# Kernel tuning notes

Measured on AMD Instinct MI355X. Metric: run time of the kernel, lower is better.

The kernel has to match this reference:

```python
import math
import jax, jax.numpy as jnp
import numpy as np

B, S, IN_DIM, D_MODEL, L, T_Y = 16, 512, 64, 64, 32, 256
T_X = T_Y + L - 1
RIDGE = 0.01
THRESH = 0.005


def _pos_encoding(seq_len, d):
    pos = jnp.arange(seq_len, dtype=jnp.float32)[:, None]
    div = jnp.exp(jnp.arange(0, d, 2, dtype=jnp.float32) * (-(math.log(10000.0) / d)))
    ang = pos * div  # [S, d/2]
    pe = jnp.zeros((seq_len, d), dtype=jnp.float32)
    pe = pe.at[:, 0::2].set(jnp.sin(ang)).at[:, 1::2].set(jnp.cos(ang))
    return pe


def _layernorm(h, gamma, beta, eps=1e-5):
    mu = jnp.mean(h, axis=-1, keepdims=True)
    var = jnp.mean((h - mu) ** 2, axis=-1, keepdims=True)
    return (h - mu) * jax.lax.rsqrt(var + eps) * gamma + beta


def setup_inputs() -> dict:
    key = jax.random.key(0)
    ks = jax.random.split(key, 8)
    return {
        "fps": jax.random.normal(ks[0], (B, S, IN_DIM), dtype=jnp.float32),
        "x": jax.random.normal(ks[1], (B, S, T_X), dtype=jnp.float32),
        "y": jax.random.normal(ks[2], (B, S, T_Y), dtype=jnp.float32),
        "sample_steps": jax.random.randint(ks[3], (5,), 10, S),
        "W1": jax.random.normal(ks[4], (IN_DIM, 256), dtype=jnp.float32) / math.sqrt(IN_DIM),
        "b1": jnp.zeros((256,), dtype=jnp.float32),
        "gamma": jnp.ones((256,), dtype=jnp.float32),
        "beta": jnp.zeros((256,), dtype=jnp.float32),
        "W2": jax.random.normal(ks[5], (256, D_MODEL), dtype=jnp.float32) / math.sqrt(256.0),
        "b2": jnp.zeros((D_MODEL,), dtype=jnp.float32),
        "Wq": jax.random.normal(ks[6], (D_MODEL, D_MODEL), dtype=jnp.float32) / math.sqrt(D_MODEL),
        "bq": jnp.zeros((D_MODEL,), dtype=jnp.float32),
        "Wk": jax.random.normal(ks[7], (D_MODEL, D_MODEL), dtype=jnp.float32) / math.sqrt(D_MODEL),
        "bk": jnp.zeros((D_MODEL,), dtype=jnp.float32),
    }


def reference(fps, x, y, sample_steps, W1, b1, gamma, beta, W2, b2, Wq, bq, Wk, bk):
    batch, seq_len, _ = fps.shape
    d = Wq.shape[0]
    t_y = y.shape[-1]
    filt = x.shape[-1] - t_y + 1  # L

    # encoder: Linear -> LayerNorm -> Tanh -> Linear -> Tanh
    h = _layernorm(fps @ W1 + b1, gamma, beta)
    e_orig = jnp.tanh(jnp.tanh(h) @ W2 + b2)  # [B,S,d]
    e = e_orig + 0.05 * _pos_encoding(seq_len, d)[None]

    q = e @ Wq + bq
    k = e @ Wk + bk
    scores = jnp.einsum('bsd,btd->bst', q, k) / math.sqrt(d)
    causal = jnp.triu(jnp.ones((seq_len, seq_len), dtype=bool), 1)
    scores = jnp.where(causal[None], -1e9, scores)
    alpha = jax.nn.softmax(scores * 2.0, axis=-1)  # [B,S,S]

    # sliding windows: X[b,s] = unfold(x[b,s], L, 1)[:T_y] -> [T_y, L]
    win = jnp.arange(t_y)[:, None] + jnp.arange(filt)[None, :]
    X = x[:, :, win]  # [B,S,T_y,L]

    # per-source gram / cross contributions
    G = jnp.einsum('bstl,bstm->bslm', X, X)  # [B,S,L,L]
    C = jnp.einsum('bstl,bst->bsl', X, y)    # [B,S,L]

    w = alpha[:, sample_steps, :]            # [B,T,S]
    wm = jnp.where(w > THRESH, w, 0.0)

    gram = jnp.einsum('bts,bslm->btlm', wm, G) + RIDGE * jnp.eye(filt, dtype=x.dtype)
    cross = jnp.einsum('bts,bsl->btl', wm, C)
    wt_hat = jnp.linalg.solve(gram, cross[..., None])[..., 0]  # [B,T,L]

    Xt = X[:, sample_steps]  # [B,T,T_y,L]
    yt = y[:, sample_steps]  # [B,T,T_y]
    pred = jnp.einsum('btkl,btl->btk', Xt, wt_hat)
    loss_bt = jnp.mean((yt - pred) ** 2, axis=-1)  # [B,T]

    valid = jnp.any(wm > 0.0, axis=-1)  # [B,T]
    total = jnp.sum(jnp.where(valid, loss_bt, 0.0))
    n = jnp.maximum(jnp.sum(valid.astype(jnp.int32)), 1)
    loss = total / n
    return loss, alpha, e_orig
```

## Files before the change

kernel.cpp:

```cpp
#include <hip/hip_runtime.h>
#include <hip/hip_bf16.h>
#include <math.h>

#define BB 16
#define SS 512
#define INDIM 64
#define DMODEL 64
#define HID 256
#define FILT 32
#define TYY 256
#define TXX 287
#define NT 5
#define RIDGEF 0.01f
#define THRESHF 0.005f
#define GRAMN 1088
#define GRAMTOT (BB * NT * GRAMN)

__global__ __launch_bounds__(256) void k_mlp(
    const float* __restrict__ fps, const float* __restrict__ W1, const float* __restrict__ b1,
    const float* __restrict__ gamma, const float* __restrict__ beta,
    const float* __restrict__ W2, const float* __restrict__ b2,
    const float* __restrict__ Wq, const float* __restrict__ bq,
    const float* __restrict__ Wk, const float* __restrict__ bk,
    float* __restrict__ e_out, float* __restrict__ q_out, float* __restrict__ kT_out,
    float* __restrict__ gram, int* __restrict__ ctrs)
{
    const int row0 = blockIdx.x << 3;
    const int tid = threadIdx.x;
    const int wid = tid >> 6, lane = tid & 63;

    if (blockIdx.x < GRAMTOT / 256) {
        gram[(size_t)blockIdx.x * 256 + tid] = 0.f;
    } else if (blockIdx.x == GRAMTOT / 256 && tid < 4) {
        ctrs[tid] = 0;
    }

    __shared__ float fr[8][INDIM];
    __shared__ float th4[8][HID];
    __shared__ float ee4[4][DMODEL];
    __shared__ float part4[4][4][DMODEL];
    __shared__ float partk4[4][4][DMODEL];
    __shared__ float wred[4][8][2];

    { int r = tid >> 6, i = tid & 63;
      fr[r][i]     = fps[(row0 + r) * INDIM + i];
      fr[r + 4][i] = fps[(row0 + r + 4) * INDIM + i]; }
    __syncthreads();

    float h[8];
    float b1v = b1[tid];
    #pragma unroll
    for (int r = 0; r < 8; ++r) h[r] = b1v;
    for (int i = 0; i < INDIM; ++i) {
        float w = W1[i * HID + tid];
        #pragma unroll
        for (int r = 0; r < 8; ++r) h[r] = fmaf(fr[r][i], w, h[r]);
    }

    float s1[8], s2[8];
    #pragma unroll
    for (int r = 0; r < 8; ++r) { s1[r] = h[r]; s2[r] = h[r] * h[r]; }
    #pragma unroll
    for (int off = 1; off < 64; off <<= 1) {
        #pragma unroll
        for (int r = 0; r < 8; ++r) {
            s1[r] += __shfl_xor(s1[r], off);
            s2[r] += __shfl_xor(s2[r], off);
        }
    }
    if (lane == 0) {
        #pragma unroll
        for (int r = 0; r < 8; ++r) { wred[wid][r][0] = s1[r]; wred[wid][r][1] = s2[r]; }
    }
    __syncthreads();
    float gm = gamma[tid], bt = beta[tid];
    #pragma unroll
    for (int r = 0; r < 8; ++r) {
        float t1 = wred[0][r][0] + wred[1][r][0] + wred[2][r][0] + wred[3][r][0];
        float t2 = wred[0][r][1] + wred[1][r][1] + wred[2][r][1] + wred[3][r][1];
        float mu = t1 * (1.0f / HID);
        float var = t2 * (1.0f / HID) - mu * mu;
        float hn = (h[r] - mu) * rsqrtf(var + 1e-5f) * gm + bt;
        th4[r][tid] = tanhf(hn);
    }
    __syncthreads();

    #pragma unroll
    for (int half = 0; half < 2; ++half) {
        const int rbase = half * 4;
        { int p = tid >> 6, j = tid & 63;
          float acc[4] = {0.f, 0.f, 0.f, 0.f};
          for (int i = p * 64; i < p * 64 + 64; ++i) {
              float w = W2[i * DMODEL + j];
              #pragma unroll
              for (int r = 0; r < 4; ++r) acc[r] = fmaf(th4[rbase + r][i], w, acc[r]);
          }
          #pragma unroll
          for (int r = 0; r < 4; ++r) part4[p][r][j] = acc[r];
        }
        __syncthreads();
        { int r = tid >> 6, j = tid & 63;
          float e = part4[0][r][j] + part4[1][r][j] + part4[2][r][j] + part4[3][r][j] + b2[j];
          float eo = tanhf(e);
          int row = row0 + rbase + r;
          int s = row & (SS - 1);
          e_out[(size_t)row * DMODEL + j] = eo;
          float div = expf(-(float)(j & ~1) * 0.14391156831212787f);
          float ang = (float)s * div;
          float pe = (j & 1) ? cosf(ang) : sinf(ang);
          ee4[r][j] = eo + 0.05f * pe;
        }
        __syncthreads();
        { int p = tid >> 6, j = tid & 63;
          float aq[4] = {0.f,0.f,0.f,0.f}, ak[4] = {0.f,0.f,0.f,0.f};
          for (int i = p * 16; i < p * 16 + 16; ++i) {
              float wqv = Wq[i * DMODEL + j];
              float wkv = Wk[i * DMODEL + j];
              #pragma unroll
              for (int r = 0; r < 4; ++r) {
                  aq[r] = fmaf(ee4[r][i], wqv, aq[r]);
                  ak[r] = fmaf(ee4[r][i], wkv, ak[r]);
              }
          }
          #pragma unroll
          for (int r = 0; r < 4; ++r) { part4[p][r][j] = aq[r]; partk4[p][r][j] = ak[r]; }
        }
        __syncthreads();
        { int r = tid >> 6, j = tid & 63;
          float qv = part4[0][r][j] + part4[1][r][j] + part4[2][r][j] + part4[3][r][j] + bq[j];
          float kv = partk4[0][r][j] + partk4[1][r][j] + partk4[2][r][j] + partk4[3][r][j] + bk[j];
          int row = row0 + rbase + r;
          int b = row >> 9, s = row & (SS - 1);
          q_out[(size_t)row * DMODEL + j] = qv;
          kT_out[(size_t)(b * DMODEL + j) * SS + s] = kv;
        }
        __syncthreads();
    }
}

__global__ __launch_bounds__(256) void k_attn(
    const float* __restrict__ q, const float* __restrict__ kT,
    float* __restrict__ alpha)
{
    const int blk = blockIdx.x;
    const int b = blk >> 7;
    const int t0 = (blk & 127) << 2;
    const int t3 = t0 + 3;
    const int tid = threadIdx.x;
    const int wave = tid >> 6, lane = tid & 63;

    __shared__ float qt[4 * DMODEL];
    __shared__ float redm[4][4];

    qt[tid] = q[(size_t)(b * SS + t0 + (tid >> 6)) * DMODEL + (tid & 63)];
    __syncthreads();

    const float* kTb = kT + (size_t)b * DMODEL * SS;
    const int s0 = tid, s1 = tid + 256;
    float a0[4] = {0,0,0,0}, a1[4] = {0,0,0,0};
    if (s1 <= t3) {
        for (int d = 0; d < DMODEL; ++d) {
            float k0 = kTb[d * SS + s0];
            float k1 = kTb[d * SS + s1];
            #pragma unroll
            for (int r = 0; r < 4; ++r) {
                float qv = qt[r * DMODEL + d];
                a0[r] = fmaf(qv, k0, a0[r]);
                a1[r] = fmaf(qv, k1, a1[r]);
            }
        }
    } else if (s0 <= t3) {
        for (int d = 0; d < DMODEL; ++d) {
            float k0 = kTb[d * SS + s0];
            #pragma unroll
            for (int r = 0; r < 4; ++r) a0[r] = fmaf(qt[r * DMODEL + d], k0, a0[r]);
        }
    }
    float lg0[4], lg1[4];
    #pragma unroll
    for (int r = 0; r < 4; ++r) {
        int tr = t0 + r;
        lg0[r] = (s0 <= tr) ? 0.25f * a0[r] : -INFINITY;
        lg1[r] = (s1 <= tr) ? 0.25f * a1[r] : -INFINITY;
    }
    float mr[4];
    #pragma unroll
    for (int r = 0; r < 4; ++r) {
        float m = fmaxf(lg0[r], lg1[r]);
        #pragma unroll
        for (int off = 32; off > 0; off >>= 1) m = fmaxf(m, __shfl_xor(m, off));
        if (lane == 0) redm[r][wave] = m;
    }
    __syncthreads();
    #pragma unroll
    for (int r = 0; r < 4; ++r)
        mr[r] = fmaxf(fmaxf(redm[r][0], redm[r][1]), fmaxf(redm[r][2], redm[r][3]));
    __syncthreads();
    float ex0[4], ex1[4], sr[4];
    #pragma unroll
    for (int r = 0; r < 4; ++r) {
        ex0[r] = expf(lg0[r] - mr[r]);
        ex1[r] = expf(lg1[r] - mr[r]);
        float sm = ex0[r] + ex1[r];
        #pragma unroll
        for (int off = 32; off > 0; off >>= 1) sm += __shfl_xor(sm, off);
        if (lane == 0) redm[r][wave] = sm;
    }
    __syncthreads();
    #pragma unroll
    for (int r = 0; r < 4; ++r)
        sr[r] = redm[r][0] + redm[r][1] + redm[r][2] + redm[r][3];
    #pragma unroll
    for (int r = 0; r < 4; ++r) {
        float inv = 1.0f / sr[r];
        size_t base = (size_t)(b * SS + t0 + r) * SS;
        alpha[base + s0] = ex0[r] * inv;
        alpha[base + s1] = ex1[r] * inv;
    }
}

__global__ __launch_bounds__(256) void k_gpart(
    const float* __restrict__ x, const float* __restrict__ y,
    const int* __restrict__ steps, const float* __restrict__ alpha,
    float* __restrict__ gram, int C, int CS)
{
    const int b = blockIdx.x / C;
    const int chunk = blockIdx.x % C;
    const int tid = threadIdx.x;
    const int lane = tid & 63, wid = tid >> 6;

    __shared__ __align__(16) float xs[288];
    __shared__ __align__(16) float ys[256];
    __shared__ float Gs[1056];
    __shared__ float crossL[32];
    __shared__ float wv[NT * 64];
    __shared__ float wtot[NT];
    __shared__ int sl[64];
    __shared__ int nselS;
    __shared__ int stS[NT];
    __shared__ float redA[4][33];
    __shared__ float redB[4][33];

    if (tid < NT) stS[tid] = steps[tid];
    if (tid < 32) Gs[tid * 33 + 32] = 0.f;
    __syncthreads();

    for (int idx = tid; idx < NT * CS; idx += 256) {
        int t = idx / CS, si = idx % CS;
        float a = alpha[(size_t)(b * SS + stS[t]) * SS + chunk * CS + si];
        wv[t * 64 + si] = (a > THRESHF) ? a : 0.f;
    }
    __syncthreads();
    if (tid < NT) {
        float s = 0.f;
        for (int si = 0; si < CS; ++si) s += wv[tid * 64 + si];
        wtot[tid] = s;
    }
    if (wid == 0) {
        float m = 0.f;
        if (lane < CS)
            m = wv[lane] + wv[64 + lane] + wv[128 + lane] + wv[192 + lane] + wv[256 + lane];
        unsigned long long mask = __ballot(m > 0.f);
        if (m > 0.f) {
            int pos = __popcll(mask & ((1ull << lane) - 1ull));
            sl[pos] = lane;
        }
        if (lane == 0) nselS = __popcll(mask);
    }
    __syncthreads();
    const int nsel = nselS;

    float acc[NT][5];
    #pragma unroll
    for (int t = 0; t < NT; ++t) {
        #pragma unroll
        for (int r = 0; r < 5; ++r) acc[t][r] = 0.f;
    }

    float rx0 = 0.f, rx1 = 0.f, ry = 0.f;
    if (nsel > 0) {
        int sg = chunk * CS + sl[0];
        const float* xr = x + (size_t)(b * SS + sg) * TXX;
        const float* yr = y + (size_t)(b * SS + sg) * TYY;
        rx0 = xr[tid];
        if (tid < 31) rx1 = xr[256 + tid];
        ry = yr[tid];
    }

    for (int i = 0; i < nsel; ++i) {
        xs[tid] = rx0;
        if (tid < 31) xs[256 + tid] = rx1;
        ys[tid] = ry;
        const int sl_cur = sl[i];
        __syncthreads();

        if (i + 1 < nsel) {
            int sg = chunk * CS + sl[i + 1];
            const float* xr = x + (size_t)(b * SS + sg) * TXX;
            const float* yr = y + (size_t)(b * SS + sg) * TYY;
            rx0 = xr[tid];
            if (tid < 31) rx1 = xr[256 + tid];
            ry = yr[tid];
        }

        { int l = tid & 31, p = tid >> 5;
          const float4* xk4 = (const float4*)(xs + (p << 5));
          const float4* yk4 = (const float4*)(ys + (p << 5));
          float c = 0.f, a = 0.f;
          #pragma unroll
          for (int j = 0; j < 8; ++j) {
              float4 xk = xk4[j];
              float4 yk = yk4[j];
              int kb = (p << 5) + (j << 2);
              float x0 = xs[kb + l],     x1 = xs[kb + 1 + l];
              float x2 = xs[kb + 2 + l], x3 = xs[kb + 3 + l];
              c = fmaf(x0, yk.x, c); a = fmaf(xk.x, x0, a);
              c = fmaf(x1, yk.y, c); a = fmaf(xk.y, x1, a);
              c = fmaf(x2, yk.z, c); a = fmaf(xk.z, x2, a);
              c = fmaf(x3, yk.w, c); a = fmaf(xk.w, x3, a);
          }
          c += __shfl_xor(c, 32);
          a += __shfl_xor(a, 32);
          if (lane < 32) { redA[wid][l] = c; redB[wid][l] = a; }
        }
        __syncthreads();

        if (tid < 32)
            crossL[tid] = redA[0][tid] + redA[1][tid] + redA[2][tid] + redA[3][tid];

        { int jj = lane & 31;
          #pragma unroll
          for (int pass = 0; pass < 4; ++pass) {
              int dd = 2 * (wid + 4 * pass) + (lane >> 5);
              float g0 = redB[0][dd] + redB[1][dd] + redB[2][dd] + redB[3][dd];
              float dlt = 0.f;
              if (jj > 0 && jj + dd < 32)
                  dlt = xs[jj + 255] * xs[jj + 255 + dd]
                      - xs[jj - 1] * xs[jj - 1 + dd];
              #pragma unroll
              for (int off = 1; off < 32; off <<= 1) {
                  float tsh = __shfl_up(dlt, off, 32);
                  if (jj >= off) dlt += tsh;
              }
              if (jj + dd < 32) {
                  float gval = g0 + dlt;
                  Gs[jj * 33 + jj + dd] = gval;
                  Gs[(jj + dd) * 33 + jj] = gval;
              }
          }
        }
        __syncthreads();

        { float g0 = Gs[tid], g1 = Gs[tid + 256], g2 = Gs[tid + 512], g3 = Gs[tid + 768];
          float g4 = (tid < 32) ? Gs[1024 + tid]
                   : ((tid < 64) ? crossL[tid - 32] : 0.f);
          #pragma unroll
          for (int t = 0; t < NT; ++t) {
              float w = wv[t * 64 + sl_cur];
              if (w > 0.f) {
                  acc[t][0] = fmaf(w, g0, acc[t][0]);
                  acc[t][1] = fmaf(w, g1, acc[t][1]);
                  acc[t][2] = fmaf(w, g2, acc[t][2]);
                  acc[t][3] = fmaf(w, g3, acc[t][3]);
                  acc[t][4] = fmaf(w, g4, acc[t][4]);
              }
          }
        }
    }

    #pragma unroll
    for (int t = 0; t < NT; ++t) {
        if (wtot[t] > 0.f) {
            float* gr = gram + (size_t)(b * NT + t) * GRAMN;
            #pragma unroll
            for (int r = 0; r < 4; ++r) atomicAdd(&gr[tid + 256 * r], acc[t][r]);
            if (tid < 64) atomicAdd(&gr[1024 + tid], acc[t][4]);
        }
    }
}

__global__ __launch_bounds__(256) void k_solve2(
    const float* __restrict__ x, const float* __restrict__ y,
    const int* __restrict__ steps, const float* __restrict__ alpha,
    const float* __restrict__ gram,
    int* __restrict__ ctrs, float* __restrict__ out0)
{
    const int g = blockIdx.x;
    const int b = g / NT, t = g % NT;
    const int tid = threadIdx.x;

    __shared__ float Af[1056];
    __shared__ float zs[FILT];
    __shared__ float wt[FILT];
    __shared__ float xsr[TXX + 1];
    __shared__ float red[256];
    __shared__ int step_s;
    __shared__ int anyv;

    if (tid == 0) { step_s = steps[t]; anyv = 0; }
    __syncthreads();

    const float* row = gram + (size_t)g * GRAMN;
    Af[tid] = row[tid];
    Af[tid + 256] = row[tid + 256];
    Af[tid + 512] = row[tid + 512];
    Af[tid + 768] = row[tid + 768];
    if (tid < 32) Af[1024 + tid] = row[1024 + tid];
    else if (tid < 64) zs[tid - 32] = row[1024 + tid];

    { const float* arow = alpha + (size_t)(b * SS + step_s) * SS;
      if (arow[tid] > THRESHF || arow[tid + 256] > THRESHF) anyv = 1; }
    __syncthreads();
    if (tid < 32) Af[tid * 33 + tid] += RIDGEF;
    __syncthreads();

    if (tid < 32) {
        float a[32];
        #pragma unroll
        for (int j = 0; j < 32; ++j) a[j] = Af[tid * 33 + j];
        #pragma unroll
        for (int k = 0; k < 32; ++k) {
            float akk = __shfl(a[k], k);
            float dk = sqrtf(akk);
            float ck = a[k] / dk;
            if (tid >= k) a[k] = ck;
            #pragma unroll
            for (int m = k + 1; m < 32; ++m) {
                float cm = __shfl(ck, m);
                if (tid >= m) a[m] = fmaf(-ck, cm, a[m]);
            }
        }
        #pragma unroll
        for (int j = 0; j < 32; ++j)
            if (j <= tid) Af[tid * 33 + j] = a[j];

        float zl = zs[tid];
        #pragma unroll
        for (int k = 0; k < 32; ++k) {
            float akk = __shfl(a[k], k);
            float zk = __shfl(zl, k) / akk;
            if (tid == k) zl = zk;
            else if (tid > k) zl = fmaf(-a[k], zk, zl);
        }
        #pragma unroll
        for (int k = 31; k >= 0; --k) {
            float akk = __shfl(a[k], k);
            float wk = __shfl(zl, k) / akk;
            if (tid == k) zl = wk;
            else if (tid < k) zl = fmaf(-Af[k * 33 + tid], wk, zl);
        }
        wt[tid] = zl;
    }
    __syncthreads();

    const int sstep = step_s;
    const float* xrow = x + (size_t)(b * SS + sstep) * TXX;
    for (int i = tid; i < TXX; i += 256) xsr[i] = xrow[i];
    __syncthreads();
    float pk = 0.f;
    #pragma unroll
    for (int l = 0; l < FILT; ++l) pk = fmaf(xsr[tid + l], wt[l], pk);
    float d = y[(size_t)(b * SS + sstep) * TYY + tid] - pk;
    red[tid] = d * d;
    __syncthreads();
    for (int off = 128; off > 0; off >>= 1) {
        if (tid < off) red[tid] += red[tid + off];
        __syncthreads();
    }
    if (tid == 0) {
        float lossval = red[0] * (1.0f / TYY);
        float* loss_sum = (float*)(ctrs + 2);
        if (anyv) {
            atomicAdd(loss_sum, lossval);
            atomicAdd(&ctrs[1], 1);
        }
        __threadfence();
        int prev = atomicAdd(&ctrs[0], 1);
        if (prev == BB * NT - 1) {
            float s = atomicAdd(loss_sum, 0.0f);
            int c = atomicAdd(&ctrs[1], 0);
            out0[0] = s / (float)(c > 0 ? c : 1);
        }
    }
}

extern "C" void kernel_launch(void* const* d_in, const int* in_sizes, int n_in,
                              void* d_out, int out_size, void* d_ws, size_t ws_size,
                              hipStream_t stream)
{
    const float* fps  = (const float*)d_in[0];
    const float* x    = (const float*)d_in[1];
    const float* y    = (const float*)d_in[2];
    const int* steps  = (const int*)d_in[3];
    const float* W1   = (const float*)d_in[4];
    const float* b1   = (const float*)d_in[5];
    const float* gamma= (const float*)d_in[6];
    const float* beta = (const float*)d_in[7];
    const float* W2   = (const float*)d_in[8];
    const float* b2   = (const float*)d_in[9];
    const float* Wq   = (const float*)d_in[10];
    const float* bq   = (const float*)d_in[11];
    const float* Wk   = (const float*)d_in[12];
    const float* bk   = (const float*)d_in[13];

    float* out   = (float*)d_out;
    float* alpha = out + 1;
    float* e_out = out + 1 + (size_t)BB * SS * SS;

    float* gram = (float*)d_ws;
    int*   ctrs = (int*)(gram + GRAMTOT);
    float* q    = (float*)(ctrs + 4);
    float* kT   = q + (size_t)BB * SS * DMODEL;

    const int C = 64, CS = SS / 64;

    hipLaunchKernelGGL(k_mlp, dim3(BB * SS / 8), dim3(256), 0, stream,
                       fps, W1, b1, gamma, beta, W2, b2, Wq, bq, Wk, bk,
                       e_out, q, kT, gram, ctrs);
    hipLaunchKernelGGL(k_attn, dim3(BB * (SS / 4)), dim3(256), 0, stream,
                       q, kT, alpha);
    hipLaunchKernelGGL(k_gpart, dim3(BB * C), dim3(256), 0, stream,
                       x, y, steps, alpha, gram, C, CS);
    hipLaunchKernelGGL(k_solve2, dim3(BB * NT), dim3(256), 0, stream,
                       x, y, steps, alpha, gram, ctrs, out);
}
```

Measured before the change: 200.2 us.

## Fuse all stages into one persistent kernel with software grid barriers

Merges the MLP, attention, gram-accumulation and solve kernels into a single persistent kernel of 448 blocks. Each block loops over work units, and the stages are separated by atomic-counter grid barriers. Zeroing of the gram buffer, counters and barriers moves to a hipMemsetAsync. The aim is to remove inter-kernel launch gaps and tail effects, at the cost of spin-wait barriers, a fixed grid that must fit co-resident (launch bounds 256,2), and a union of shared-memory layouts.

```diff
diff --git a/kernel.cpp b/kernel.cpp
--- a/kernel.cpp
+++ b/kernel.cpp
@@ -1,5 +1,4 @@
 #include <hip/hip_runtime.h>
-#include <hip/hip_bf16.h>
 #include <math.h>
 
 #define BB 16
@@ -15,287 +14,294 @@
 #define THRESHF 0.005f
 #define GRAMN 1088
 #define GRAMTOT (BB * NT * GRAMN)
-
-__global__ __launch_bounds__(256) void k_mlp(
-    const float* __restrict__ fps, const float* __restrict__ W1, const float* __restrict__ b1,
+#define NBLK 448
+
+union __align__(16) SharedU {
+    struct {
+        float fr[8][INDIM];
+        float th4[8][HID];
+        float ee4[4][DMODEL];
+        float part4[4][4][DMODEL];
+        float partk4[4][4][DMODEL];
+        float wred[4][8][2];
+    } m;
+    struct {
+        float qt[4 * DMODEL];
+        float redm[4][4];
+    } a;
+    struct {
+        float xs[288];
+        float ys[256];
+        float Gs[1056];
+        float crossL[32];
+        float wv[NT * 64];
+        float wtot[NT];
+        int sl[64];
+        int nselS;
+        int stS[NT];
+        float redA[4][33];
+        float redB[4][33];
+    } g;
+    struct {
+        float Af[1056];
+        float zs[FILT];
+        float wt[FILT];
+        float xsr[TXX + 1];
+        float red[256];
+    } s;
+};
+
+__device__ __forceinline__ void grid_barrier(int* bar2, int nblocks)
+{
+    __syncthreads();
+    if (threadIdx.x == 0) {
+        __threadfence();
+        if (atomicAdd(&bar2[0], 1) == nblocks - 1) {
+            atomicExch(&bar2[1], 1);
+        } else {
+            while (atomicAdd(&bar2[1], 0) == 0) __builtin_amdgcn_s_sleep(8);
+        }
+        __threadfence();
+    }
+    __syncthreads();
+}
+
+__global__ __launch_bounds__(256, 2) void k_fused(
+    const float* __restrict__ fps, const float* __restrict__ x,
+    const float* __restrict__ y, const int* __restrict__ steps,
+    const float* __restrict__ W1, const float* __restrict__ b1,
     const float* __restrict__ gamma, const float* __restrict__ beta,
     const float* __restrict__ W2, const float* __restrict__ b2,
     const float* __restrict__ Wq, const float* __restrict__ bq,
     const float* __restrict__ Wk, const float* __restrict__ bk,
-    float* __restrict__ e_out, float* __restrict__ q_out, float* __restrict__ kT_out,
-    float* __restrict__ gram, int* __restrict__ ctrs)
+    float* __restrict__ e_out, float* __restrict__ alpha,
+    float* __restrict__ q_out, float* __restrict__ kT_out,
+    float* __restrict__ gram, int* __restrict__ ctrs, int* __restrict__ bars,
+    float* __restrict__ out0)
 {
-    const int row0 = blockIdx.x << 3;
+    __shared__ SharedU su;
     const int tid = threadIdx.x;
     const int wid = tid >> 6, lane = tid & 63;
 
-    if (blockIdx.x < GRAMTOT / 256) {
-        gram[(size_t)blockIdx.x * 256 + tid] = 0.f;
-    } else if (blockIdx.x == GRAMTOT / 256 && tid < 4) {
-        ctrs[tid] = 0;
+    for (int u = blockIdx.x; u < BB * SS / 8; u += NBLK) {
+        const int row0 = u << 3;
+        { int r = tid >> 6, i = tid & 63;
+          su.m.fr[r][i]     = fps[(row0 + r) * INDIM + i];
+          su.m.fr[r + 4][i] = fps[(row0 + r + 4) * INDIM + i]; }
+        __syncthreads();
+
+        float h[8];
+        float b1v = b1[tid];
+        #pragma unroll
+        for (int r = 0; r < 8; ++r) h[r] = b1v;
+        for (int i = 0; i < INDIM; ++i) {
+            float w = W1[i * HID + tid];
+            #pragma unroll
+            for (int r = 0; r < 8; ++r) h[r] = fmaf(su.m.fr[r][i], w, h[r]);
+        }
+
+        float s1[8], s2[8];
+        #pragma unroll
+        for (int r = 0; r < 8; ++r) { s1[r] = h[r]; s2[r] = h[r] * h[r]; }
+        #pragma unroll
+        for (int off = 1; off < 64; off <<= 1) {
+            #pragma unroll
+            for (int r = 0; r < 8; ++r) {
+                s1[r] += __shfl_xor(s1[r], off);
+                s2[r] += __shfl_xor(s2[r], off);
+            }
+        }
+        if (lane == 0) {
+            #pragma unroll
+            for (int r = 0; r < 8; ++r) { su.m.wred[wid][r][0] = s1[r]; su.m.wred[wid][r][1] = s2[r]; }
+        }
+        __syncthreads();
+        float gm = gamma[tid], bt = beta[tid];
+        #pragma unroll
+        for (int r = 0; r < 8; ++r) {
+            float t1 = su.m.wred[0][r][0] + su.m.wred[1][r][0] + su.m.wred[2][r][0] + su.m.wred[3][r][0];
+            float t2 = su.m.wred[0][r][1] + su.m.wred[1][r][1] + su.m.wred[2][r][1] + su.m.wred[3][r][1];
+            float mu = t1 * (1.0f / HID);
+            float var = t2 * (1.0f / HID) - mu * mu;
+            float hn = (h[r] - mu) * rsqrtf(var + 1e-5f) * gm + bt;
+            su.m.th4[r][tid] = tanhf(hn);
+        }
+        __syncthreads();
+
+        #pragma unroll
+        for (int half = 0; half < 2; ++half) {
+            const int rbase = half * 4;
+            { int p = tid >> 6, j = tid & 63;
+              float acc[4] = {0.f, 0.f, 0.f, 0.f};
+              for (int i = p * 64; i < p * 64 + 64; ++i) {
+                  float w = W2[i * DMODEL + j];
+                  #pragma unroll
+                  for (int r = 0; r < 4; ++r) acc[r] = fmaf(su.m.th4[rbase + r][i], w, acc[r]);
+              }
+              #pragma unroll
+              for (int r = 0; r < 4; ++r) su.m.part4[p][r][j] = acc[r];
+            }
+            __syncthreads();
+            { int r = tid >> 6, j = tid & 63;
+              float e = su.m.part4[0][r][j] + su.m.part4[1][r][j] + su.m.part4[2][r][j] + su.m.part4[3][r][j] + b2[j];
+              float eo = tanhf(e);
+              int row = row0 + rbase + r;
+              int s = row & (SS - 1);
+              e_out[(size_t)row * DMODEL + j] = eo;
+              float div = expf(-(float)(j & ~1) * 0.14391156831212787f);
+              float ang = (float)s * div;
+              float pe = (j & 1) ? cosf(ang) : sinf(ang);
+              su.m.ee4[r][j] = eo + 0.05f * pe;
+            }
+            __syncthreads();
+            { int p = tid >> 6, j = tid & 63;
+              float aq[4] = {0.f,0.f,0.f,0.f}, ak[4] = {0.f,0.f,0.f,0.f};
+              for (int i = p * 16; i < p * 16 + 16; ++i) {
+                  float wqv = Wq[i * DMODEL + j];
+                  float wkv = Wk[i * DMODEL + j];
+                  #pragma unroll
+                  for (int r = 0; r < 4; ++r) {
+                      aq[r] = fmaf(su.m.ee4[r][i], wqv, aq[r]);
+                      ak[r] = fmaf(su.m.ee4[r][i], wkv, ak[r]);
+                  }
+              }
+              #pragma unroll
+              for (int r = 0; r < 4; ++r) { su.m.part4[p][r][j] = aq[r]; su.m.partk4[p][r][j] = ak[r]; }
+            }
+            __syncthreads();
+            { int r = tid >> 6, j = tid & 63;
+              float qv = su.m.part4[0][r][j] + su.m.part4[1][r][j] + su.m.part4[2][r][j] + su.m.part4[3][r][j] + bq[j];
+              float kv = su.m.partk4[0][r][j] + su.m.partk4[1][r][j] + su.m.partk4[2][r][j] + su.m.partk4[3][r][j] + bk[j];
+              int row = row0 + rbase + r;
+              int b = row >> 9, s = row & (SS - 1);
+              q_out[(size_t)row * DMODEL + j] = qv;
+              kT_out[(size_t)(b * DMODEL + j) * SS + s] = kv;
+            }
+            __syncthreads();
+        }
     }
-
-    __shared__ float fr[8][INDIM];
-    __shared__ float th4[8][HID];
-    __shared__ float ee4[4][DMODEL];
-    __shared__ float part4[4][4][DMODEL];
-    __shared__ float partk4[4][4][DMODEL];
-    __shared__ float wred[4][8][2];
-
-    { int r = tid >> 6, i = tid & 63;
-      fr[r][i]     = fps[(row0 + r) * INDIM + i];
-      fr[r + 4][i] = fps[(row0 + r + 4) * INDIM + i]; }
-    __syncthreads();
-
-    float h[8];
-    float b1v = b1[tid];
-    #pragma unroll
-    for (int r = 0; r < 8; ++r) h[r] = b1v;
-    for (int i = 0; i < INDIM; ++i) {
-        float w = W1[i * HID + tid];
-        #pragma unroll
-        for (int r = 0; r < 8; ++r) h[r] = fmaf(fr[r][i], w, h[r]);
+    grid_barrier(bars + 0, NBLK);
+
+    for (int u = blockIdx.x; u < BB * (SS / 4); u += NBLK) {
+        const int b = u >> 7;
+        const int t0 = (u & 127) << 2;
+        const int t3 = t0 + 3;
+
+        su.a.qt[tid] = q_out[(size_t)(b * SS + t0 + (tid >> 6)) * DMODEL + (tid & 63)];
+        __syncthreads();
+
+        const float* kTb = kT_out + (size_t)b * DMODEL * SS;
+        const int s0 = tid, s1 = tid + 256;
+        float a0[4] = {0,0,0,0}, a1[4] = {0,0,0,0};
+        if (s1 <= t3) {
+            for (int d = 0; d < DMODEL; ++d) {
+                float k0 = kTb[d * SS + s0];
+                float k1 = kTb[d * SS + s1];
+                #pragma unroll
+                for (int r = 0; r < 4; ++r) {
+                    float qv = su.a.qt[r * DMODEL + d];
+                    a0[r] = fmaf(qv, k0, a0[r]);
+                    a1[r] = fmaf(qv, k1, a1[r]);
+                }
+            }
+        } else if (s0 <= t3) {
+            for (int d = 0; d < DMODEL; ++d) {
+                float k0 = kTb[d * SS + s0];
+                #pragma unroll
+                for (int r = 0; r < 4; ++r) a0[r] = fmaf(su.a.qt[r * DMODEL + d], k0, a0[r]);
+            }
+        }
+        float lg0[4], lg1[4];
+        #pragma unroll
+        for (int r = 0; r < 4; ++r) {
+            int tr = t0 + r;
+            lg0[r] = (s0 <= tr) ? 0.25f * a0[r] : -INFINITY;
+            lg1[r] = (s1 <= tr) ? 0.25f * a1[r] : -INFINITY;
+        }
+        float mr[4];
+        #pragma unroll
+        for (int r = 0; r < 4; ++r) {
+            float m = fmaxf(lg0[r], lg1[r]);
+            #pragma unroll
+            for (int off = 32; off > 0; off >>= 1) m = fmaxf(m, __shfl_xor(m, off));
+            if (lane == 0) su.a.redm[r][wid] = m;
+        }
+        __syncthreads();
+        #pragma unroll
+        for (int r = 0; r < 4; ++r)
+            mr[r] = fmaxf(fmaxf(su.a.redm[r][0], su.a.redm[r][1]),
+                          fmaxf(su.a.redm[r][2], su.a.redm[r][3]));
+        __syncthreads();
+        float ex0[4], ex1[4], sr[4];
+        #pragma unroll
+        for (int r = 0; r < 4; ++r) {
+            ex0[r] = expf(lg0[r] - mr[r]);
+            ex1[r] = expf(lg1[r] - mr[r]);
+            float sm = ex0[r] + ex1[r];
+            #pragma unroll
+            for (int off = 32; off > 0; off >>= 1) sm += __shfl_xor(sm, off);
+            if (lane == 0) su.a.redm[r][wid] = sm;
+        }
+        __syncthreads();
+        #pragma unroll
+        for (int r = 0; r < 4; ++r)
+            sr[r] = su.a.redm[r][0] + su.a.redm[r][1] + su.a.redm[r][2] + su.a.redm[r][3];
+        #pragma unroll
+        for (int r = 0; r < 4; ++r) {
+            float inv = 1.0f / sr[r];
+            size_t base = (size_t)(b * SS + t0 + r) * SS;
+            alpha[base + s0] = ex0[r] * inv;
+            alpha[base + s1] = ex1[r] * inv;
+        }
+        __syncthreads();
     }
-
-    float s1[8], s2[8];
-    #pragma unroll
-    for (int r = 0; r < 8; ++r) { s1[r] = h[r]; s2[r] = h[r] * h[r]; }
-    #pragma unroll
-    for (int off = 1; off < 64; off <<= 1) {
-        #pragma unroll
-        for (int r = 0; r < 8; ++r) {
-            s1[r] += __shfl_xor(s1[r], off);
-            s2[r] += __shfl_xor(s2[r], off);
-        }
-    }
-    if (lane == 0) {
-        #pragma unroll
-        for (int r = 0; r < 8; ++r) { wred[wid][r][0] = s1[r]; wred[wid][r][1] = s2[r]; }
-    }
-    __syncthreads();
-    float gm = gamma[tid], bt = beta[tid];
-    #pragma unroll
-    for (int r = 0; r < 8; ++r) {
-        float t1 = wred[0][r][0] + wred[1][r][0] + wred[2][r][0] + wred[3][r][0];
-        float t2 = wred[0][r][1] + wred[1][r][1] + wred[2][r][1] + wred[3][r][1];
-        float mu = t1 * (1.0f / HID);
-        float var = t2 * (1.0f / HID) - mu * mu;
-        float hn = (h[r] - mu) * rsqrtf(var + 1e-5f) * gm + bt;
-        th4[r][tid] = tanhf(hn);
-    }
-    __syncthreads();
-
-    #pragma unroll
-    for (int half = 0; half < 2; ++half) {
-        const int rbase = half * 4;
-        { int p = tid >> 6, j = tid & 63;
-          float acc[4] = {0.f, 0.f, 0.f, 0.f};
-          for (int i = p * 64; i < p * 64 + 64; ++i) {
-              float w = W2[i * DMODEL + j];
-              #pragma unroll
-              for (int r = 0; r < 4; ++r) acc[r] = fmaf(th4[rbase + r][i], w, acc[r]);
-          }
-          #pragma unroll
-          for (int r = 0; r < 4; ++r) part4[p][r][j] = acc[r];
-        }
-        __syncthreads();
-        { int r = tid >> 6, j = tid & 63;
-          float e = part4[0][r][j] + part4[1][r][j] + part4[2][r][j] + part4[3][r][j] + b2[j];
-          float eo = tanhf(e);
-          int row = row0 + rbase + r;
-          int s = row & (SS - 1);
-          e_out[(size_t)row * DMODEL + j] = eo;
-          float div = expf(-(float)(j & ~1) * 0.14391156831212787f);
-          float ang = (float)s * div;
-          float pe = (j & 1) ? cosf(ang) : sinf(ang);
-          ee4[r][j] = eo + 0.05f * pe;
-        }
-        __syncthreads();
-        { int p = tid >> 6, j = tid & 63;
-          float aq[4] = {0.f,0.f,0.f,0.f}, ak[4] = {0.f,0.f,0.f,0.f};
-          for (int i = p * 16; i < p * 16 + 16; ++i) {
-              float wqv = Wq[i * DMODEL + j];
-              float wkv = Wk[i * DMODEL + j];
-              #pragma unroll
-              for (int r = 0; r < 4; ++r) {
-                  aq[r] = fmaf(ee4[r][i], wqv, aq[r]);
-                  ak[r] = fmaf(ee4[r][i], wkv, ak[r]);
-              }
-          }
-          #pragma unroll
-          for (int r = 0; r < 4; ++r) { part4[p][r][j] = aq[r]; partk4[p][r][j] = ak[r]; }
-        }
-        __syncthreads();
-        { int r = tid >> 6, j = tid & 63;
-          float qv = part4[0][r][j] + part4[1][r][j] + part4[2][r][j] + part4[3][r][j] + bq[j];
-          float kv = partk4[0][r][j] + partk4[1][r][j] + partk4[2][r][j] + partk4[3][r][j] + bk[j];
-          int row = row0 + rbase + r;
-          int b = row >> 9, s = row & (SS - 1);
-          q_out[(size_t)row * DMODEL + j] = qv;
-          kT_out[(size_t)(b * DMODEL + j) * SS + s] = kv;
-        }
-        __syncthreads();
-    }
-}
-
-__global__ __launch_bounds__(256) void k_attn(
-    const float* __restrict__ q, const float* __restrict__ kT,
-    float* __restrict__ alpha)
-{
-    const int blk = blockIdx.x;
-    const int b = blk >> 7;
-    const int t0 = (blk & 127) << 2;
-    const int t3 = t0 + 3;
-    const int tid = threadIdx.x;
-    const int wave = tid >> 6, lane = tid & 63;
-
-    __shared__ float qt[4 * DMODEL];
-    __shared__ float redm[4][4];
-
-    qt[tid] = q[(size_t)(b * SS + t0 + (tid >> 6)) * DMODEL + (tid & 63)];
-    __syncthreads();
-
-    const float* kTb = kT + (size_t)b * DMODEL * SS;
-    const int s0 = tid, s1 = tid + 256;
-    float a0[4] = {0,0,0,0}, a1[4] = {0,0,0,0};
-    if (s1 <= t3) {
-        for (int d = 0; d < DMODEL; ++d) {
-            float k0 = kTb[d * SS + s0];
-            float k1 = kTb[d * SS + s1];
-            #pragma unroll
-            for (int r = 0; r < 4; ++r) {
-                float qv = qt[r * DMODEL + d];
-                a0[r] = fmaf(qv, k0, a0[r]);
-                a1[r] = fmaf(qv, k1, a1[r]);
-            }
-        }
-    } else if (s0 <= t3) {
-        for (int d = 0; d < DMODEL; ++d) {
-            float k0 = kTb[d * SS + s0];
-            #pragma unroll
-            for (int r = 0; r < 4; ++r) a0[r] = fmaf(qt[r * DMODEL + d], k0, a0[r]);
-        }
-    }
-    float lg0[4], lg1[4];
-    #pragma unroll
-    for (int r = 0; r < 4; ++r) {
-        int tr = t0 + r;
-        lg0[r] = (s0 <= tr) ? 0.25f * a0[r] : -INFINITY;
-        lg1[r] = (s1 <= tr) ? 0.25f * a1[r] : -INFINITY;
-    }
-    float mr[4];
-    #pragma unroll
-    for (int r = 0; r < 4; ++r) {
-        float m = fmaxf(lg0[r], lg1[r]);
-        #pragma unroll
-        for (int off = 32; off > 0; off >>= 1) m = fmaxf(m, __shfl_xor(m, off));
-        if (lane == 0) redm[r][wave] = m;
-    }
-    __syncthreads();
-    #pragma unroll
-    for (int r = 0; r < 4; ++r)
-        mr[r] = fmaxf(fmaxf(redm[r][0], redm[r][1]), fmaxf(redm[r][2], redm[r][3]));
-    __syncthreads();
-    float ex0[4], ex1[4], sr[4];
-    #pragma unroll
-    for (int r = 0; r < 4; ++r) {
-        ex0[r] = expf(lg0[r] - mr[r]);
-        ex1[r] = expf(lg1[r] - mr[r]);
-        float sm = ex0[r] + ex1[r];
-        #pragma unroll
-        for (int off = 32; off > 0; off >>= 1) sm += __shfl_xor(sm, off);
-        if (lane == 0) redm[r][wave] = sm;
-    }
-    __syncthreads();
-    #pragma unroll
-    for (int r = 0; r < 4; ++r)
-        sr[r] = redm[r][0] + redm[r][1] + redm[r][2] + redm[r][3];
-    #pragma unroll
-    for (int r = 0; r < 4; ++r) {
-        float inv = 1.0f / sr[r];
-        size_t base = (size_t)(b * SS + t0 + r) * SS;
-        alpha[base + s0] = ex0[r] * inv;
-        alpha[base + s1] = ex1[r] * inv;
-    }
-}
-
-__global__ __launch_bounds__(256) void k_gpart(
-    const float* __restrict__ x, const float* __restrict__ y,
-    const int* __restrict__ steps, const float* __restrict__ alpha,
-    float* __restrict__ gram, int C, int CS)
-{
-    const int b = blockIdx.x / C;
-    const int chunk = blockIdx.x % C;
-    const int tid = threadIdx.x;
-    const int lane = tid & 63, wid = tid >> 6;
-
-    __shared__ __align__(16) float xs[288];
-    __shared__ __align__(16) float ys[256];
-    __shared__ float Gs[1056];
-    __shared__ float crossL[32];
-    __shared__ float wv[NT * 64];
-    __shared__ float wtot[NT];
-    __shared__ int sl[64];
-    __shared__ int nselS;
-    __shared__ int stS[NT];
-    __shared__ float redA[4][33];
-    __shared__ float redB[4][33];
-
-    if (tid < NT) stS[tid] = steps[tid];
-    if (tid < 32) Gs[tid * 33 + 32] = 0.f;
-    __syncthreads();
-
-    for (int idx = tid; idx < NT * CS; idx += 256) {
-        int t = idx / CS, si = idx % CS;
-        float a = alpha[(size_t)(b * SS + stS[t]) * SS + chunk * CS + si];
-        wv[t * 64 + si] = (a > THRESHF) ? a : 0.f;
-    }
-    __syncthreads();
-    if (tid < NT) {
-        float s = 0.f;
-        for (int si = 0; si < CS; ++si) s += wv[tid * 64 + si];
-        wtot[tid] = s;
-    }
-    if (wid == 0) {
-        float m = 0.f;
-        if (lane < CS)
-            m = wv[lane] + wv[64 + lane] + wv[128 + lane] + wv[192 + lane] + wv[256 + lane];
-        unsigned long long mask = __ballot(m > 0.f);
-        if (m > 0.f) {
-            int pos = __popcll(mask & ((1ull << lane) - 1ull));
-            sl[pos] = lane;
-        }
-        if (lane == 0) nselS = __popcll(mask);
-    }
-    __syncthreads();
-    const int nsel = nselS;
-
-    float acc[NT][5];
-    #pragma unroll
-    for (int t = 0; t < NT; ++t) {
-        #pragma unroll
-        for (int r = 0; r < 5; ++r) acc[t][r] = 0.f;
-    }
-
-    float rx0 = 0.f, rx1 = 0.f, ry = 0.f;
-    if (nsel > 0) {
-        int sg = chunk * CS + sl[0];
-        const float* xr = x + (size_t)(b * SS + sg) * TXX;
-        const float* yr = y + (size_t)(b * SS + sg) * TYY;
-        rx0 = xr[tid];
-        if (tid < 31) rx1 = xr[256 + tid];
-        ry = yr[tid];
-    }
-
-    for (int i = 0; i < nsel; ++i) {
-        xs[tid] = rx0;
-        if (tid < 31) xs[256 + tid] = rx1;
-        ys[tid] = ry;
-        const int sl_cur = sl[i];
-        __syncthreads();
-
-        if (i + 1 < nsel) {
-            int sg = chunk * CS + sl[i + 1];
+    grid_barrier(bars + 2, NBLK);
+
+    const int C = 64, CS = SS / 64;
+    for (int u = blockIdx.x; u < BB * C; u += NBLK) {
+        const int b = u / C;
+        const int chunk = u % C;
+
+        if (tid < NT) su.g.stS[tid] = steps[tid];
+        if (tid < 32) su.g.Gs[tid * 33 + 32] = 0.f;
+        __syncthreads();
+
+        for (int idx = tid; idx < NT * CS; idx += 256) {
+            int t = idx / CS, si = idx % CS;
+            float a = alpha[(size_t)(b * SS + su.g.stS[t]) * SS + chunk * CS + si];
+            su.g.wv[t * 64 + si] = (a > THRESHF) ? a : 0.f;
+        }
+        __syncthreads();
+        if (tid < NT) {
+            float s = 0.f;
+            for (int si = 0; si < CS; ++si) s += su.g.wv[tid * 64 + si];
+            su.g.wtot[tid] = s;
+        }
+        if (wid == 0) {
+            float m = 0.f;
+            if (lane < CS)
+                m = su.g.wv[lane] + su.g.wv[64 + lane] + su.g.wv[128 + lane]
+                  + su.g.wv[192 + lane] + su.g.wv[256 + lane];
+            unsigned long long mask = __ballot(m > 0.f);
+            if (m > 0.f) {
+                int pos = __popcll(mask & ((1ull << lane) - 1ull));
+                su.g.sl[pos] = lane;
+            }
+            if (lane == 0) su.g.nselS = __popcll(mask);
+        }
+        __syncthreads();
+        const int nsel = su.g.nselS;
+
+        float acc[NT][5];
+        #pragma unroll
+        for (int t = 0; t < NT; ++t) {
+            #pragma unroll
+            for (int r = 0; r < 5; ++r) acc[t][r] = 0.f;
+        }
+
+        float rx0 = 0.f, rx1 = 0.f, ry = 0.f;
+        if (nsel > 0) {
+            int sg = chunk * CS + su.g.sl[0];
             const float* xr = x + (size_t)(b * SS + sg) * TXX;
             const float* yr = y + (size_t)(b * SS + sg) * TYY;
             rx0 = xr[tid];
@@ -303,184 +309,194 @@
             ry = yr[tid];
         }
 
-        { int l = tid & 31, p = tid >> 5;
-          const float4* xk4 = (const float4*)(xs + (p << 5));
-          const float4* yk4 = (const float4*)(ys + (p << 5));
-          float c = 0.f, a = 0.f;
+        for (int i = 0; i < nsel; ++i) {
+            su.g.xs[tid] = rx0;
+            if (tid < 31) su.g.xs[256 + tid] = rx1;
+            su.g.ys[tid] = ry;
+            const int sl_cur = su.g.sl[i];
+            __syncthreads();
+
+            if (i + 1 < nsel) {
+                int sg = chunk * CS + su.g.sl[i + 1];
+                const float* xr = x + (size_t)(b * SS + sg) * TXX;
+                const float* yr = y + (size_t)(b * SS + sg) * TYY;
+                rx0 = xr[tid];
+                if (tid < 31) rx1 = xr[256 + tid];
+                ry = yr[tid];
+            }
+
+            { int l = tid & 31, p = tid >> 5;
+              const float4* xk4 = (const float4*)(su.g.xs + (p << 5));
+              const float4* yk4 = (const float4*)(su.g.ys + (p << 5));
+              float c = 0.f, a = 0.f;
+              #pragma unroll
+              for (int j = 0; j < 8; ++j) {
+                  float4 xk = xk4[j];
+                  float4 yk = yk4[j];
+                  int kb = (p << 5) + (j << 2);
+                  float x0 = su.g.xs[kb + l],     x1 = su.g.xs[kb + 1 + l];
+                  float x2 = su.g.xs[kb + 2 + l], x3 = su.g.xs[kb + 3 + l];
+                  c = fmaf(x0, yk.x, c); a = fmaf(xk.x, x0, a);
+                  c = fmaf(x1, yk.y, c); a = fmaf(xk.y, x1, a);
+                  c = fmaf(x2, yk.z, c); a = fmaf(xk.z, x2, a);
+                  c = fmaf(x3, yk.w, c); a = fmaf(xk.w, x3, a);
+              }
+              c += __shfl_xor(c, 32);
+              a += __shfl_xor(a, 32);
+              if (lane < 32) { su.g.redA[wid][l] = c; su.g.redB[wid][l] = a; }
+            }
+            __syncthreads();
+
+            if (tid < 32)
+                su.g.crossL[tid] = su.g.redA[0][tid] + su.g.redA[1][tid]
+                                 + su.g.redA[2][tid] + su.g.redA[3][tid];
+
+            { int jj = lane & 31;
+              #pragma unroll
+              for (int pass = 0; pass < 4; ++pass) {
+                  int dd = 2 * (wid + 4 * pass) + (lane >> 5);
+                  float g0 = su.g.redB[0][dd] + su.g.redB[1][dd]
+                           + su.g.redB[2][dd] + su.g.redB[3][dd];
+                  float dlt = 0.f;
+                  if (jj > 0 && jj + dd < 32)
+                      dlt = su.g.xs[jj + 255] * su.g.xs[jj + 255 + dd]
+                          - su.g.xs[jj - 1] * su.g.xs[jj - 1 + dd];
+                  #pragma unroll
+                  for (int off = 1; off < 32; off <<= 1) {
+                      float tsh = __shfl_up(dlt, off, 32);
+                      if (jj >= off) dlt += tsh;
+                  }
+                  if (jj + dd < 32) {
+                      float gval = g0 + dlt;
+                      su.g.Gs[jj * 33 + jj + dd] = gval;
+                      su.g.Gs[(jj + dd) * 33 + jj] = gval;
+                  }
+              }
+            }
+            __syncthreads();
+
+            { float g0 = su.g.Gs[tid], g1 = su.g.Gs[tid + 256];
+              float g2 = su.g.Gs[tid + 512], g3 = su.g.Gs[tid + 768];
+              float g4 = (tid < 32) ? su.g.Gs[1024 + tid]
+                       : ((tid < 64) ? su.g.crossL[tid - 32] : 0.f);
+              #pragma unroll
+              for (int t = 0; t < NT; ++t) {
+                  float w = su.g.wv[t * 64 + sl_cur];
+                  if (w > 0.f) {
+                      acc[t][0] = fmaf(w, g0, acc[t][0]);
+                      acc[t][1] = fmaf(w, g1, acc[t][1]);
+                      acc[t][2] = fmaf(w, g2, acc[t][2]);
+                      acc[t][3] = fmaf(w, g3, acc[t][3]);
+                      acc[t][4] = fmaf(w, g4, acc[t][4]);
+                  }
+              }
+            }
+        }
+
+        #pragma unroll
+        for (int t = 0; t < NT; ++t) {
+            if (su.g.wtot[t] > 0.f) {
+                float* gr = gram + (size_t)(b * NT + t) * GRAMN;
+                #pragma unroll
+                for (int r = 0; r < 4; ++r) atomicAdd(&gr[tid + 256 * r], acc[t][r]);
+                if (tid < 64) atomicAdd(&gr[1024 + tid], acc[t][4]);
+            }
+        }
+        __syncthreads();
+    }
+    grid_barrier(bars + 4, NBLK);
+
+    for (int g = blockIdx.x; g < BB * NT; g += NBLK) {
+        const int b = g / NT, t = g % NT;
+        const int step_s = steps[t];
+
+        const float* row = gram + (size_t)g * GRAMN;
+        su.s.Af[tid] = row[tid];
+        su.s.Af[tid + 256] = row[tid + 256];
+        su.s.Af[tid + 512] = row[tid + 512];
+        su.s.Af[tid + 768] = row[tid + 768];
+        if (tid < 32) su.s.Af[1024 + tid] = row[1024 + tid];
+        else if (tid < 64) su.s.zs[tid - 32] = row[1024 + tid];
+
+        int anyv = 0;
+        { const float* arow = alpha + (size_t)(b * SS + step_s) * SS;
+          anyv = (arow[tid] > THRESHF || arow[tid + 256] > THRESHF) ? 1 : 0;
           #pragma unroll
-          for (int j = 0; j < 8; ++j) {
-              float4 xk = xk4[j];
-              float4 yk = yk4[j];
-              int kb = (p << 5) + (j << 2);
-              float x0 = xs[kb + l],     x1 = xs[kb + 1 + l];
-              float x2 = xs[kb + 2 + l], x3 = xs[kb + 3 + l];
-              c = fmaf(x0, yk.x, c); a = fmaf(xk.x, x0, a);
-              c = fmaf(x1, yk.y, c); a = fmaf(xk.y, x1, a);
-              c = fmaf(x2, yk.z, c); a = fmaf(xk.z, x2, a);
-              c = fmaf(x3, yk.w, c); a = fmaf(xk.w, x3, a);
-          }
-          c += __shfl_xor(c, 32);
-          a += __shfl_xor(a, 32);
-          if (lane < 32) { redA[wid][l] = c; redB[wid][l] = a; }
-        }
-        __syncthreads();
-
-        if (tid < 32)
-            crossL[tid] = redA[0][tid] + redA[1][tid] + redA[2][tid] + redA[3][tid];
-
-        { int jj = lane & 31;
-          #pragma unroll
-          for (int pass = 0; pass < 4; ++pass) {
-              int dd = 2 * (wid + 4 * pass) + (lane >> 5);
-              float g0 = redB[0][dd] + redB[1][dd] + redB[2][dd] + redB[3][dd];
-              float dlt = 0.f;
-              if (jj > 0 && jj + dd < 32)
-                  dlt = xs[jj + 255] * xs[jj + 255 + dd]
-                      - xs[jj - 1] * xs[jj - 1 + dd];
-              #pragma unroll
-              for (int off = 1; off < 32; off <<= 1) {
-                  float tsh = __shfl_up(dlt, off, 32);
-                  if (jj >= off) dlt += tsh;
-              }
-              if (jj + dd < 32) {
-                  float gval = g0 + dlt;
-                  Gs[jj * 33 + jj + dd] = gval;
-                  Gs[(jj + dd) * 33 + jj] = gval;
-              }
-          }
-        }
-        __syncthreads();
-
-        { float g0 = Gs[tid], g1 = Gs[tid + 256], g2 = Gs[tid + 512], g3 = Gs[tid + 768];
-          float g4 = (tid < 32) ? Gs[1024 + tid]
-                   : ((tid < 64) ? crossL[tid - 32] : 0.f);
-          #pragma unroll
-          for (int t = 0; t < NT; ++t) {
-              float w = wv[t * 64 + sl_cur];
-              if (w > 0.f) {
-                  acc[t][0] = fmaf(w, g0, acc[t][0]);
-                  acc[t][1] = fmaf(w, g1, acc[t][1]);
-                  acc[t][2] = fmaf(w, g2, acc[t][2]);
-                  acc[t][3] = fmaf(w, g3, acc[t][3]);
-                  acc[t][4] = fmaf(w, g4, acc[t][4]);
-              }
-          }
-        }
-    }
-
-    #pragma unroll
-    for (int t = 0; t < NT; ++t) {
-        if (wtot[t] > 0.f) {
-            float* gr = gram + (size_t)(b * NT + t) * GRAMN;
-            #pragma unroll
-            for (int r = 0; r < 4; ++r) atomicAdd(&gr[tid + 256 * r], acc[t][r]);
-            if (tid < 64) atomicAdd(&gr[1024 + tid], acc[t][4]);
-        }
-    }
-}
-
-__global__ __launch_bounds__(256) void k_solve2(
-    const float* __restrict__ x, const float* __restrict__ y,
-    const int* __restrict__ steps, const float* __restrict__ alpha,
-    const float* __restrict__ gram,
-    int* __restrict__ ctrs, float* __restrict__ out0)
-{
-    const int g = blockIdx.x;
-    const int b = g / NT, t = g % NT;
-    const int tid = threadIdx.x;
-
-    __shared__ float Af[1056];
-    __shared__ float zs[FILT];
-    __shared__ float wt[FILT];
-    __shared__ float xsr[TXX + 1];
-    __shared__ float red[256];
-    __shared__ int step_s;
-    __shared__ int anyv;
-
-    if (tid == 0) { step_s = steps[t]; anyv = 0; }
-    __syncthreads();
-
-    const float* row = gram + (size_t)g * GRAMN;
-    Af[tid] = row[tid];
-    Af[tid + 256] = row[tid + 256];
-    Af[tid + 512] = row[tid + 512];
-    Af[tid + 768] = row[tid + 768];
-    if (tid < 32) Af[1024 + tid] = row[1024 + tid];
-    else if (tid < 64) zs[tid - 32] = row[1024 + tid];
-
-    { const float* arow = alpha + (size_t)(b * SS + step_s) * SS;
-      if (arow[tid] > THRESHF || arow[tid + 256] > THRESHF) anyv = 1; }
-    __syncthreads();
-    if (tid < 32) Af[tid * 33 + tid] += RIDGEF;
-    __syncthreads();
-
-    if (tid < 32) {
-        float a[32];
-        #pragma unroll
-        for (int j = 0; j < 32; ++j) a[j] = Af[tid * 33 + j];
-        #pragma unroll
-        for (int k = 0; k < 32; ++k) {
-            float akk = __shfl(a[k], k);
-            float dk = sqrtf(akk);
-            float ck = a[k] / dk;
-            if (tid >= k) a[k] = ck;
-            #pragma unroll
-            for (int m = k + 1; m < 32; ++m) {
-                float cm = __shfl(ck, m);
-                if (tid >= m) a[m] = fmaf(-ck, cm, a[m]);
-            }
-        }
-        #pragma unroll
-        for (int j = 0; j < 32; ++j)
-            if (j <= tid) Af[tid * 33 + j] = a[j];
-
-        float zl = zs[tid];
-        #pragma unroll
-        for (int k = 0; k < 32; ++k) {
-            float akk = __shfl(a[k], k);
-            float zk = __shfl(zl, k) / akk;
-            if (tid == k) zl = zk;
-            else if (tid > k) zl = fmaf(-a[k], zk, zl);
-        }
-        #pragma unroll
-        for (int k = 31; k >= 0; --k) {
-            float akk = __shfl(a[k], k);
-            float wk = __shfl(zl, k) / akk;
-            if (tid == k) zl = wk;
-            else if (tid < k) zl = fmaf(-Af[k * 33 + tid], wk, zl);
-        }
-        wt[tid] = zl;
-    }
-    __syncthreads();
-
-    const int sstep = step_s;
-    const float* xrow = x + (size_t)(b * SS + sstep) * TXX;
-    for (int i = tid; i < TXX; i += 256) xsr[i] = xrow[i];
-    __syncthreads();
-    float pk = 0.f;
-    #pragma unroll
-    for (int l = 0; l < FILT; ++l) pk = fmaf(xsr[tid + l], wt[l], pk);
-    float d = y[(size_t)(b * SS + sstep) * TYY + tid] - pk;
-    red[tid] = d * d;
-    __syncthreads();
-    for (int off = 128; off > 0; off >>= 1) {
-        if (tid < off) red[tid] += red[tid + off];
-        __syncthreads();
-    }
-    if (tid == 0) {
-        float lossval = red[0] * (1.0f / TYY);
-        float* loss_sum = (float*)(ctrs + 2);
-        if (anyv) {
-            atomicAdd(loss_sum, lossval);
-            atomicAdd(&ctrs[1], 1);
-        }
-        __threadfence();
-        int prev = atomicAdd(&ctrs[0], 1);
-        if (prev == BB * NT - 1) {
-            float s = atomicAdd(loss_sum, 0.0f);
-            int c = atomicAdd(&ctrs[1], 0);
-            out0[0] = s / (float)(c > 0 ? c : 1);
-        }
+          for (int off = 32; off > 0; off >>= 1) anyv |= __shfl_xor(anyv, off);
+          if (lane == 0) su.s.red[wid] = (float)anyv; }
+        __syncthreads();
+        anyv = (su.s.red[0] + su.s.red[1] + su.s.red[2] + su.s.red[3]) > 0.f;
+        if (tid < 32) su.s.Af[tid * 33 + tid] += RIDGEF;
+        __syncthreads();
+
+        if (tid < 32) {
+            float a[32];
+            #pragma unroll
+            for (int j = 0; j < 32; ++j) a[j] = su.s.Af[tid * 33 + j];
+            #pragma unroll
+            for (int k = 0; k < 32; ++k) {
+                float akk = __shfl(a[k], k);
+                float dk = sqrtf(akk);
+                float ck = a[k] / dk;
+                if (tid >= k) a[k] = ck;
+                #pragma unroll
+                for (int m = k + 1; m < 32; ++m) {
+                    float cm = __shfl(ck, m);
+                    if (tid >= m) a[m] = fmaf(-ck, cm, a[m]);
+                }
+            }
+            #pragma unroll
+            for (int j = 0; j < 32; ++j)
+                if (j <= tid) su.s.Af[tid * 33 + j] = a[j];
+
+            float zl = su.s.zs[tid];
+            #pragma unroll
+            for (int k = 0; k < 32; ++k) {
+                float akk = __shfl(a[k], k);
+                float zk = __shfl(zl, k) / akk;
+                if (tid == k) zl = zk;
+                else if (tid > k) zl = fmaf(-a[k], zk, zl);
+            }
+            #pragma unroll
+            for (int k = 31; k >= 0; --k) {
+                float akk = __shfl(a[k], k);
+                float wk = __shfl(zl, k) / akk;
+                if (tid == k) zl = wk;
+                else if (tid < k) zl = fmaf(-su.s.Af[k * 33 + tid], wk, zl);
+            }
+            su.s.wt[tid] = zl;
+        }
+        __syncthreads();
+
+        const float* xrow = x + (size_t)(b * SS + step_s) * TXX;
+        for (int i = tid; i < TXX; i += 256) su.s.xsr[i] = xrow[i];
+        __syncthreads();
+        float pk = 0.f;
+        #pragma unroll
+        for (int l = 0; l < FILT; ++l) pk = fmaf(su.s.xsr[tid + l], su.s.wt[l], pk);
+        float d = y[(size_t)(b * SS + step_s) * TYY + tid] - pk;
+        su.s.red[tid] = d * d;
+        __syncthreads();
+        for (int off = 128; off > 0; off >>= 1) {
+            if (tid < off) su.s.red[tid] += su.s.red[tid + off];
+            __syncthreads();
+        }
+        if (tid == 0) {
+            float lossval = su.s.red[0] * (1.0f / TYY);
+            float* loss_sum = (float*)(ctrs + 2);
+            if (anyv) {
+                atomicAdd(loss_sum, lossval);
+                atomicAdd(&ctrs[1], 1);
+            }
+            __threadfence();
+            int prev = atomicAdd(&ctrs[0], 1);
+            if (prev == BB * NT - 1) {
+                float s = atomicAdd(loss_sum, 0.0f);
+                int c = atomicAdd(&ctrs[1], 0);
+                out0[0] = s / (float)(c > 0 ? c : 1);
+            }
+        }
+        __syncthreads();
     }
 }
 
@@ -509,18 +525,14 @@
 
     float* gram = (float*)d_ws;
     int*   ctrs = (int*)(gram + GRAMTOT);
-    float* q    = (float*)(ctrs + 4);
+    int*   bars = ctrs + 4;
+    float* q    = (float*)d_ws + GRAMTOT + 16;
     float* kT   = q + (size_t)BB * SS * DMODEL;
 
-    const int C = 64, CS = SS / 64;
-
-    hipLaunchKernelGGL(k_mlp, dim3(BB * SS / 8), dim3(256), 0, stream,
-                       fps, W1, b1, gamma, beta, W2, b2, Wq, bq, Wk, bk,
-                       e_out, q, kT, gram, ctrs);
-    hipLaunchKernelGGL(k_attn, dim3(BB * (SS / 4)), dim3(256), 0, stream,
-                       q, kT, alpha);
-    hipLaunchKernelGGL(k_gpart, dim3(BB * C), dim3(256), 0, stream,
-                       x, y, steps, alpha, gram, C, CS);
-    hipLaunchKernelGGL(k_solve2, dim3(BB * NT), dim3(256), 0, stream,
-                       x, y, steps, alpha, gram, ctrs, out);
+    hipMemsetAsync(gram, 0, (size_t)GRAMTOT * 4 + 64, stream);
+
+    hipLaunchKernelGGL(k_fused, dim3(NBLK), dim3(256), 0, stream,
+                       fps, x, y, steps, W1, b1, gamma, beta, W2, b2,
+                       Wq, bq, Wk, bk, e_out, alpha, q, kT,
+                       gram, ctrs, bars, out);
 }
```

After: 369.9 us. 84.8% more time.
